# Performance work log

Measured on AMD Instinct MI355X. Metric: run time of the kernel, lower is better.

Reference implementation:

```python
import jax, jax.numpy as jnp
import numpy as np
from jax import lax

# dims
B, K, P, S = 16, 2048, 512, 16   # batch, votes, num_proposal, nsample
C = 256                           # seed_feat_dim
RADIUS = 0.3
NH, NS, PRE, TXT = 12, 10, 256, 10
HEAD_OUT = 5 + 2 * NH + 4 * NS + PRE  # conv3 out channels = 325


def setup_inputs() -> dict:
    key = jax.random.key(0)
    ks = jax.random.split(key, 16)
    w = lambda k, shp: jax.random.normal(k, shp, jnp.float32) * 0.05
    return {
        'xyz': jax.random.normal(ks[0], (B, K, 3), jnp.float32),
        'features': jax.random.normal(ks[1], (B, C, K), jnp.float32),
        'text_feats': jax.random.normal(ks[2], (TXT, 512), jnp.float32),
        # grouping MLP (1x1 conv2d, bias folded into BN)
        'g_w0': w(ks[3], (3 + C, 128)), 'g_w1': w(ks[4], (128, 128)), 'g_w2': w(ks[5], (128, 128)),
        'g_gam0': jnp.ones(128), 'g_bet0': jnp.zeros(128),
        'g_gam1': jnp.ones(128), 'g_bet1': jnp.zeros(128),
        'g_gam2': jnp.ones(128), 'g_bet2': jnp.zeros(128),
        # decode head
        'conv1_w': w(ks[6], (128, 128)), 'conv1_b': jnp.zeros(128),
        'bn1_g': jnp.ones(128), 'bn1_b': jnp.zeros(128),
        'conv2_w': w(ks[7], (128, 128)), 'conv2_b': jnp.zeros(128),
        'bn2_g': jnp.ones(128), 'bn2_b': jnp.zeros(128),
        'conv3_w': w(ks[8], (128, HEAD_OUT)), 'conv3_b': jnp.zeros(HEAD_OUT),
        # clip header
        'h_w0': w(ks[9], (PRE, 512)), 'h_b0': jnp.zeros(512), 'h_g0': jnp.ones(512), 'h_be0': jnp.zeros(512),
        'h_w1': w(ks[10], (512, 512)), 'h_b1': jnp.zeros(512), 'h_g1': jnp.ones(512), 'h_be1': jnp.zeros(512),
        'h_w2': w(ks[11], (512, 512)), 'h_b2': jnp.zeros(512),
    }


def _fps(pts):
    # farthest point sampling of P points from pts [K,3], starting at index 0
    Kp = pts.shape[0]
    def step(carry, _):
        dmin, last = carry
        d = jnp.sum((pts - pts[last]) ** 2, -1)
        dmin = jnp.minimum(dmin, d)
        nxt = jnp.argmax(dmin).astype(jnp.int32)
        return (dmin, nxt), nxt
    d0 = jnp.full((Kp,), 1e10, pts.dtype)
    _, rest = lax.scan(step, (d0, jnp.int32(0)), None, length=P - 1)
    return jnp.concatenate([jnp.zeros((1,), jnp.int32), rest])


def _bn(x, gam, bet):
    # training-mode batchnorm over all dims but channel (last)
    ax = tuple(range(x.ndim - 1))
    m = x.mean(ax, keepdims=True)
    v = x.var(ax, keepdims=True)
    return gam * (x - m) * lax.rsqrt(v + 1e-5) + bet


def reference(xyz, features, text_feats, g_w0, g_w1, g_w2, g_gam0, g_bet0, g_gam1, g_bet1, g_gam2, g_bet2, conv1_w, conv1_b, bn1_g, bn1_b, conv2_w, conv2_b, bn2_g, bn2_b, conv3_w, conv3_b, h_w0, h_b0, h_g0, h_be0, h_w1, h_b1, h_g1, h_be1, h_w2, h_b2):
    feats_kc = features.transpose(0, 2, 1)            # [B,K,C]
    inds = jax.vmap(_fps)(xyz)                        # [B,P] int32
    new_xyz = jnp.take_along_axis(xyz, inds[..., None], axis=1)  # [B,P,3]
    # ball query: first-S in-radius indices, pad with first valid (center itself)
    d2 = jnp.sum((new_xyz[:, :, None, :] - xyz[:, None, :, :]) ** 2, -1)  # [B,P,K]
    score = jnp.where(d2 < RADIUS * RADIUS, jnp.arange(K, dtype=jnp.int32), jnp.int32(K))
    neg_vals, idx = lax.top_k(-score, S)              # smallest valid indices first
    idx = jnp.where(neg_vals > -K, idx, idx[..., :1])  # [B,P,S]
    gather = jax.vmap(lambda pts, i: pts[i])
    gx = (gather(xyz, idx) - new_xyz[:, :, None, :]) / RADIUS  # normalize_xyz
    gf = gather(feats_kc, idx)
    g = jnp.concatenate([gx, gf], -1)                 # [B,P,S,3+C] (use_xyz)
    h = jax.nn.relu(_bn(g @ g_w0, g_gam0, g_bet0))
    h = jax.nn.relu(_bn(h @ g_w1, g_gam1, g_bet1))
    h = jax.nn.relu(_bn(h @ g_w2, g_gam2, g_bet2))
    feat = h.max(axis=2)                              # [B,P,128] max-pool over neighbors
    net = jax.nn.relu(_bn(feat @ conv1_w + conv1_b, bn1_g, bn1_b))
    net = jax.nn.relu(_bn(net @ conv2_w + conv2_b, bn2_g, bn2_b))
    net = net @ conv3_w + conv3_b                     # [B,P,325]
    clip_in = net[..., -PRE:]
    hh = jax.nn.relu(_bn(clip_in @ h_w0 + h_b0, h_g0, h_be0))
    hh = jax.nn.relu(_bn(hh @ h_w1 + h_b1, h_g1, h_be1))
    q = hh @ h_w2 + h_b2                              # [B,P,512]
    q = q / jnp.linalg.norm(q, axis=-1, keepdims=True)
    t = text_feats / jnp.linalg.norm(text_feats, axis=-1, keepdims=True)
    logits = (1.0 / 0.07) * jnp.einsum('bpd,td->bpt', q, t)  # logit_scale = exp(log(1/0.07))
    out = jnp.concatenate([net[..., :-PRE], logits], -1)     # [B,P,69+TXT]
    return out.transpose(0, 2, 1)                     # [B,79,P] like torch `net`
```

## Files before the change

### kernel.cpp

```cpp
#include <hip/hip_runtime.h>
#include <hip/hip_bf16.h>
#include <cstdint>
#include <cstddef>

#define Bb 16
#define Kk 2048
#define Pp 512
#define Ss 16
#define Cc 256

typedef __attribute__((ext_vector_type(8))) short bf16x8;
typedef __attribute__((ext_vector_type(4))) float f32x4;
typedef float v2f __attribute__((ext_vector_type(2)));

__device__ __forceinline__ unsigned short f2bf(float x) {
  unsigned u = __float_as_uint(x);
  u = (u + 0x7FFF + ((u >> 16) & 1)) >> 16;
  return (unsigned short)u;
}
__device__ __forceinline__ float bf2f(unsigned short s) {
  return __uint_as_float((unsigned)s << 16);
}
__device__ __forceinline__ void split2(float x, short& h, short& l) {
  unsigned u = __float_as_uint(x);
  h = (short)(u >> 16);
  float r = x - __uint_as_float(u & 0xFFFF0000u);
  l = (short)(__float_as_uint(r) >> 16);
}

static constexpr size_t OFF_TNORM = 0;
static constexpr size_t OFF_SUMS  = 20480;
static constexpr size_t OFF_INDS  = 36864;
static constexpr size_t OFF_IDXL  = 69632;
static constexpr size_t OFF_GX    = 593920;
static constexpr size_t OFF_F1    = 2166784;
static constexpr size_t OFF_BIGA  = 18944000;
static constexpr size_t OFF_BIGB  = 86052864;
static constexpr size_t OFF_NET   = 153161728;
static constexpr size_t OFF_WTH   = 155422720;
static constexpr size_t OFF_WTL   = 156962816;

#define WT_GW1 0
#define WT_GW2 16384
#define WT_C1  32768
#define WT_C2  49152
#define WT_H0  65536
#define WT_H1  196608
#define WT_H2  458752
#define WT_C3  720896

#define SB0S 0
#define SB0Q 128
#define SB1S 256
#define SB1Q 384
#define SB2S 512
#define SB2Q 640
#define SC1S 768
#define SC1Q 896
#define SC2S 1024
#define SC2Q 1152
#define SH0S 1280
#define SH0Q 1792
#define SH1S 2304
#define SH1Q 2816

template <int CTRL>
__device__ __forceinline__ float fmax_dpp(float v) {
  int o = __builtin_amdgcn_update_dpp(0, __float_as_int(v), CTRL, 0xF, 0xF, true);
  return fmaxf(v, __int_as_float(o));
}

__global__ __launch_bounds__(256, 1) void fused_pre(
    const float* __restrict__ xyz, int* __restrict__ inds,
    const float* __restrict__ features, const float* __restrict__ g_w0,
    float* __restrict__ F1, const float* __restrict__ text,
    float* __restrict__ tn, const float* __restrict__ g_w1,
    const float* __restrict__ g_w2, const float* __restrict__ conv1_w,
    const float* __restrict__ conv2_w, const float* __restrict__ conv3_w,
    const float* __restrict__ h_w0, const float* __restrict__ h_w1,
    const float* __restrict__ h_w2, unsigned short* __restrict__ wth,
    unsigned short* __restrict__ wtl) {
  __shared__ __align__(16) float smem[8208];
  const int tid = threadIdx.x;

  if (blockIdx.x < 16) {
    #pragma clang fp contract(off)
    const int b = blockIdx.x;
    float4* pt4 = (float4*)smem;
    unsigned long long (*redw)[4] = (unsigned long long(*)[4])(smem + 8192);
    const float* base = xyz + (size_t)b * Kk * 3;
    for (int i = tid; i < Kk; i += 256) {
      pt4[i] = make_float4(base[3 * i], base[3 * i + 1], base[3 * i + 2], 0.f);
    }
    if (tid == 0) inds[b * Pp] = 0;
    v2f PX[4], PY[4], PZ[4], DM[4];
    {
      const float* pb = base + tid * 24;
      float4 f0 = *(const float4*)(pb + 0);
      float4 f1 = *(const float4*)(pb + 4);
      float4 f2 = *(const float4*)(pb + 8);
      float4 f3 = *(const float4*)(pb + 12);
      float4 f4 = *(const float4*)(pb + 16);
      float4 f5 = *(const float4*)(pb + 20);
      PX[0] = (v2f){f0.x, f0.w}; PY[0] = (v2f){f0.y, f1.x}; PZ[0] = (v2f){f0.z, f1.y};
      PX[1] = (v2f){f1.z, f2.y}; PY[1] = (v2f){f1.w, f2.z}; PZ[1] = (v2f){f2.x, f2.w};
      PX[2] = (v2f){f3.x, f3.w}; PY[2] = (v2f){f3.y, f4.x}; PZ[2] = (v2f){f3.z, f4.y};
      PX[3] = (v2f){f4.z, f5.y}; PY[3] = (v2f){f4.w, f5.z}; PZ[3] = (v2f){f5.x, f5.w};
      #pragma unroll
      for (int p = 0; p < 4; p++) DM[p] = (v2f){1e10f, 1e10f};
    }
    __syncthreads();
    const int lane = tid & 63, wid = tid >> 6;
    int last = 0;
    for (int it = 1; it < Pp; ++it) {
      float4 L = pt4[last];
      v2f vlx = {L.x, L.x}, vly = {L.y, L.y}, vlz = {L.z, L.z};
      float pf[4];
      int pk_[4];
      #pragma unroll
      for (int p = 0; p < 4; p++) {
        v2f dx = PX[p] - vlx, dy = PY[p] - vly, dz = PZ[p] - vlz;
        v2f d = (dx * dx + dy * dy) + dz * dz;
        v2f m2 = __builtin_elementwise_min(DM[p], d);
        DM[p] = m2;
        bool t = m2.y > m2.x;
        pf[p] = t ? m2.y : m2.x;
        pk_[p] = 2 * p + (t ? 1 : 0);
      }
      bool t01 = pf[1] > pf[0];
      float f01 = t01 ? pf[1] : pf[0];
      int k01 = t01 ? pk_[1] : pk_[0];
      bool t23 = pf[3] > pf[2];
      float f23 = t23 ? pf[3] : pf[2];
      int k23 = t23 ? pk_[3] : pk_[2];
      bool tt = f23 > f01;
      float bf = tt ? f23 : f01;
      int bj = tt ? k23 : k01;
      float g = bf;
      g = fmax_dpp<0xB1>(g);
      g = fmax_dpp<0x4E>(g);
      g = fmax_dpp<0x141>(g);
      g = fmax_dpp<0x140>(g);
      g = fmax_dpp<0x142>(g);
      g = fmax_dpp<0x143>(g);
      float gs = __uint_as_float(
          (unsigned)__builtin_amdgcn_readlane(__float_as_int(g), 63));
      unsigned long long msk = __ballot(bf == gs);
      int src = __builtin_ctzll(msk);
      int kk = (tid << 3) | bj;
      int kwin = __builtin_amdgcn_readlane(kk, src);
      if (lane == 0)
        redw[it & 1][wid] = ((unsigned long long)__float_as_uint(gs) << 32) |
                            (unsigned)(~(unsigned)kwin);
      __syncthreads();
      unsigned long long q0 = redw[it & 1][0], q1 = redw[it & 1][1];
      unsigned long long q2 = redw[it & 1][2], q3 = redw[it & 1][3];
      unsigned long long m0 = q0 > q1 ? q0 : q1;
      unsigned long long m1 = q2 > q3 ? q2 : q3;
      unsigned long long mm = m0 > m1 ? m0 : m1;
      last = (int)(~(unsigned)mm);
      if (tid == 0) inds[b * Pp + it] = last;
    }
  } else if (blockIdx.x == 528) {
    int w = tid >> 6, lane = tid & 63;
    for (int r = w; r < 10; r += 4) {
      const float* rw = text + (size_t)r * 512;
      float v[8];
      float ss = 0.f;
      #pragma unroll
      for (int u = 0; u < 8; u++) { v[u] = rw[lane + 64 * u]; ss += v[u] * v[u]; }
      #pragma unroll
      for (int off = 32; off; off >>= 1) ss += __shfl_xor(ss, off, 64);
      float nrm = sqrtf(ss);
      #pragma unroll
      for (int u = 0; u < 8; u++)
        tn[(size_t)r * 512 + lane + 64 * u] = v[u] / nrm;
    }
  } else if (blockIdx.x >= 529) {
    int wb = blockIdx.x - 529;
    const float* W;
    int K, N, NS, nblk, pidx;
    unsigned short *dh, *dl;
    if (wb < 4)       { W = g_w1;    K = 128; N = 128; NS = 128; dh = wth + WT_GW1; dl = wtl + WT_GW1; nblk = 4;  pidx = wb; }
    else if (wb < 8)  { W = g_w2;    K = 128; N = 128; NS = 128; dh = wth + WT_GW2; dl = wtl + WT_GW2; nblk = 4;  pidx = wb - 4; }
    else if (wb < 12) { W = conv1_w; K = 128; N = 128; NS = 128; dh = wth + WT_C1;  dl = wtl + WT_C1;  nblk = 4;  pidx = wb - 8; }
    else if (wb < 16) { W = conv2_w; K = 128; N = 128; NS = 128; dh = wth + WT_C2;  dl = wtl + WT_C2;  nblk = 4;  pidx = wb - 12; }
    else if (wb < 32) { W = h_w0;    K = 256; N = 512; NS = 512; dh = wth + WT_H0;  dl = wtl + WT_H0;  nblk = 16; pidx = wb - 16; }
    else if (wb < 64) { W = h_w1;    K = 512; N = 512; NS = 512; dh = wth + WT_H1;  dl = wtl + WT_H1;  nblk = 32; pidx = wb - 32; }
    else if (wb < 96) { W = h_w2;    K = 512; N = 512; NS = 512; dh = wth + WT_H2;  dl = wtl + WT_H2;  nblk = 32; pidx = wb - 64; }
    else              { W = conv3_w; K = 128; N = 384; NS = 325; dh = wth + WT_C3;  dl = wtl + WT_C3;  nblk = 4;  pidx = wb - 96; }
    for (int idx = pidx * 256 + tid; idx < K * N; idx += nblk * 256) {
      int k = idx / N, n = idx - k * N;
      float w = (n < NS) ? W[k * NS + n] : 0.f;
      unsigned short hi = f2bf(w);
      unsigned short lo = f2bf(w - bf2f(hi));
      dh[n * K + k] = hi;
      dl[n * K + k] = lo;
    }
  } else {
    float (*a_t)[68] = (float(*)[68])smem;
    float (*b_t)[128] = (float(*)[128])(smem + 32 * 68);
    const float* W = g_w0 + 3 * 128;
    const int m0 = (blockIdx.x - 16) * 64;
    float acc[4][8];
    #pragma unroll
    for (int i = 0; i < 4; i++)
      #pragma unroll
      for (int j = 0; j < 8; j++) acc[i][j] = 0.f;
    const int ty = tid >> 4, tx = tid & 15;
    const int lr = tid & 63, wv = tid >> 6;
    const int bb = m0 >> 11, k0 = m0 & 2047;
    const float* fb = features + (size_t)bb * (Cc * Kk);
    for (int c0 = 0; c0 < 256; c0 += 32) {
      #pragma unroll
      for (int i = 0; i < 8; i++) {
        int c = c0 + wv + 4 * i;
        a_t[wv + 4 * i][lr] = fb[(size_t)c * Kk + k0 + lr];
      }
      #pragma unroll
      for (int p = 0; p < 4; p++) {
        int cc = p * 8 + (tid >> 5);
        int nl = (tid & 31) * 4;
        *(float4*)&b_t[cc][nl] = *(const float4*)&W[(size_t)(c0 + cc) * 128 + nl];
      }
      __syncthreads();
      #pragma unroll
      for (int kk = 0; kk < 32; kk++) {
        float4 av = *(const float4*)&a_t[kk][ty * 4];
        float4 b0 = *(const float4*)&b_t[kk][tx * 4];
        float4 b1 = *(const float4*)&b_t[kk][tx * 4 + 64];
        float ap[4] = {av.x, av.y, av.z, av.w};
        float bq0[4] = {b0.x, b0.y, b0.z, b0.w};
        float bq1[4] = {b1.x, b1.y, b1.z, b1.w};
        #pragma unroll
        for (int i = 0; i < 4; i++) {
          #pragma unroll
          for (int u = 0; u < 4; u++) {
            acc[i][u] = fmaf(ap[i], bq0[u], acc[i][u]);
            acc[i][4 + u] = fmaf(ap[i], bq1[u], acc[i][4 + u]);
          }
        }
      }
      __syncthreads();
    }
    #pragma unroll
    for (int i = 0; i < 4; i++) {
      size_t mrow = (size_t)(m0 + ty * 4 + i);
      #pragma unroll
      for (int gq = 0; gq < 2; gq++) {
        float4 v4 = make_float4(acc[i][gq * 4], acc[i][gq * 4 + 1],
                                acc[i][gq * 4 + 2], acc[i][gq * 4 + 3]);
        *(float4*)&F1[mrow * 128 + gq * 64 + tx * 4] = v4;
      }
    }
  }
}

__global__ __launch_bounds__(256) void neigh_k(
    const float* __restrict__ xyz, const int* __restrict__ inds,
    const float* __restrict__ F1, const float* __restrict__ g_w0,
    int* __restrict__ idxl, float* __restrict__ gx, float* __restrict__ s0,
    float* __restrict__ q0) {
  __shared__ float rs[128], rq[128];
  const int tid = threadIdx.x;
  if (tid < 128) { rs[tid] = 0.f; rq[tid] = 0.f; }
  __syncthreads();
  int widx = blockIdx.x * 4 + (tid >> 6);
  int lane = tid & 63;
  int b = widx >> 9;
  int q = inds[widx];
  const float* base = xyz + (size_t)b * Kk * 3;
  float qx = base[3 * q], qy = base[3 * q + 1], qz = base[3 * q + 2];
  int cnt = 0;
  int myk = 0;
  for (int ch = 0; ch < 32 && cnt < Ss; ch++) {
    int k = ch * 64 + lane;
    float dx = base[3 * k] - qx;
    float dy = base[3 * k + 1] - qy;
    float dz = base[3 * k + 2] - qz;
    float d2 = __fadd_rn(__fadd_rn(__fmul_rn(dx, dx), __fmul_rn(dy, dy)),
                         __fmul_rn(dz, dz));
    unsigned long long m = __ballot(d2 < 0.09f);
    while (m && cnt < Ss) {
      int t = __builtin_ctzll(m);
      if (lane == cnt) myk = ch * 64 + t;
      cnt++;
      m &= m - 1;
    }
  }
  int first = __shfl(myk, 0, 64);
  int kksel = 0;
  float g0r = 0.f, g1r = 0.f, g2r = 0.f;
  if (lane < Ss) {
    int kk = (lane < cnt) ? myk : first;
    kksel = kk;
    g0r = (base[3 * kk] - qx) / 0.3f;
    g1r = (base[3 * kk + 1] - qy) / 0.3f;
    g2r = (base[3 * kk + 2] - qz) / 0.3f;
    size_t o = (size_t)widx * Ss + lane;
    idxl[o] = kk;
    gx[o * 3 + 0] = g0r;
    gx[o * 3 + 1] = g1r;
    gx[o * 3 + 2] = g2r;
  }
  const float* f1b = F1 + (size_t)(b << 11) * 128;
  float wa0 = g_w0[lane], wa1 = g_w0[128 + lane], wa2 = g_w0[256 + lane];
  float wb0 = g_w0[64 + lane], wb1 = g_w0[192 + lane], wb2 = g_w0[320 + lane];
  float sa = 0.f, qa = 0.f, sb = 0.f, qb = 0.f;
  #pragma unroll
  for (int s = 0; s < Ss; s++) {
    int bidx = __shfl(kksel, s, 64);
    float gg0 = __shfl(g0r, s, 64);
    float gg1 = __shfl(g1r, s, 64);
    float gg2 = __shfl(g2r, s, 64);
    const float* fr = f1b + (size_t)bidx * 128;
    float va = fr[lane] + gg0 * wa0 + gg1 * wa1 + gg2 * wa2;
    float vb = fr[64 + lane] + gg0 * wb0 + gg1 * wb1 + gg2 * wb2;
    sa += va; qa += va * va;
    sb += vb; qb += vb * vb;
  }
  atomicAdd(&rs[lane], sa);
  atomicAdd(&rq[lane], qa);
  atomicAdd(&rs[64 + lane], sb);
  atomicAdd(&rq[64 + lane], qb);
  __syncthreads();
  if (tid < 128) {
    atomicAdd(&s0[tid], rs[tid]);
    atomicAdd(&q0[tid], rq[tid]);
  }
}

template <int KD, bool INBN, bool HASBIAS, bool OSUM, bool OMAX, bool WCLIP,
          bool ABF16, bool GATHER, bool OBF16>
__global__ __launch_bounds__(256, 2) void gemm_mfma(
    const void* __restrict__ A, const unsigned short* __restrict__ Wh,
    const unsigned short* __restrict__ Wl, const float* __restrict__ bias,
    const float* __restrict__ isum, const float* __restrict__ isq,
    float inv_cnt, const float* __restrict__ gamma,
    const float* __restrict__ beta, void* __restrict__ outp, int N, int nout,
    float* __restrict__ clipf, float* __restrict__ osum,
    float* __restrict__ osq, const int* __restrict__ idxl,
    const float* __restrict__ gxv, const float* __restrict__ w0raw) {
  __shared__ float sc[INBN ? KD : 1];
  __shared__ float sh[INBN ? KD : 1];
  __shared__ float red_s[OSUM ? 128 : 1];
  __shared__ float red_q[OSUM ? 128 : 1];
  const int tid = threadIdx.x;
  if (INBN) {
    for (int c = tid; c < KD; c += 256) {
      float mean = isum[c] * inv_cnt;
      float var = isq[c] * inv_cnt - mean * mean;
      float is_ = rsqrtf(var + 1e-5f);
      float scl = gamma[c] * is_;
      sc[c] = scl;
      sh[c] = beta[c] - mean * scl;
    }
  }
  if (OSUM && tid < 128) { red_s[tid] = 0.f; red_q[tid] = 0.f; }
  __syncthreads();
  const int wave = tid >> 6, lane = tid & 63;
  const int wm = wave >> 1, wn = wave & 1;
  const int r = lane & 15, g = lane >> 4;
  const size_t m0 = (size_t)blockIdx.x * 128 + wm * 64;
  const int n0 = blockIdx.y * 128 + wn * 64;

  const float* Af = (const float*)A;
  const unsigned short* Ab = (const unsigned short*)A;

  size_t gi[4];
  float gx0[4], gx1[4], gx2[4];
  if (GATHER) {
    #pragma unroll
    for (int mf = 0; mf < 4; mf++) {
      int row = (int)m0 + mf * 16 + r;
      gi[mf] = ((size_t)((row >> 13) << 11) + idxl[row]) * 128;
      gx0[mf] = gxv[3 * (size_t)row];
      gx1[mf] = gxv[3 * (size_t)row + 1];
      gx2[mf] = gxv[3 * (size_t)row + 2];
    }
  }

  f32x4 acc[4][4] = {};
  for (int ks = 0; ks < KD / 32; ks++) {
    const int kb = ks * 32 + g * 8;
    bf16x8 bh[4], bl[4];
    #pragma unroll
    for (int nf = 0; nf < 4; nf++) {
      bh[nf] = *(const bf16x8*)&Wh[(size_t)(n0 + nf * 16 + r) * KD + kb];
      bl[nf] = *(const bf16x8*)&Wl[(size_t)(n0 + nf * 16 + r) * KD + kb];
    }
    float s8[8], h8[8];
    if (INBN) {
      #pragma unroll
      for (int j = 0; j < 8; j++) { s8[j] = sc[kb + j]; h8[j] = sh[kb + j]; }
    }
    float wxr[8], wyr[8], wzr[8];
    if (GATHER) {
      float4 a0 = *(const float4*)&w0raw[kb];
      float4 a1 = *(const float4*)&w0raw[kb + 4];
      float4 b0 = *(const float4*)&w0raw[128 + kb];
      float4 b1 = *(const float4*)&w0raw[128 + kb + 4];
      float4 c0 = *(const float4*)&w0raw[256 + kb];
      float4 c1 = *(const float4*)&w0raw[256 + kb + 4];
      wxr[0]=a0.x; wxr[1]=a0.y; wxr[2]=a0.z; wxr[3]=a0.w;
      wxr[4]=a1.x; wxr[5]=a1.y; wxr[6]=a1.z; wxr[7]=a1.w;
      wyr[0]=b0.x; wyr[1]=b0.y; wyr[2]=b0.z; wyr[3]=b0.w;
      wyr[4]=b1.x; wyr[5]=b1.y; wyr[6]=b1.z; wyr[7]=b1.w;
      wzr[0]=c0.x; wzr[1]=c0.y; wzr[2]=c0.z; wzr[3]=c0.w;
      wzr[4]=c1.x; wzr[5]=c1.y; wzr[6]=c1.z; wzr[7]=c1.w;
    }
    #pragma unroll
    for (int mf = 0; mf < 4; mf++) {
      float xv[8];
      if (GATHER) {
        const float* fp = Af + gi[mf] + kb;
        float4 x0 = *(const float4*)fp;
        float4 x1 = *(const float4*)(fp + 4);
        xv[0]=x0.x; xv[1]=x0.y; xv[2]=x0.z; xv[3]=x0.w;
        xv[4]=x1.x; xv[5]=x1.y; xv[6]=x1.z; xv[7]=x1.w;
        #pragma unroll
        for (int j = 0; j < 8; j++)
          xv[j] += gx0[mf] * wxr[j] + gx1[mf] * wyr[j] + gx2[mf] * wzr[j];
      } else if (ABF16) {
        bf16x8 rawv = *(const bf16x8*)&Ab[(m0 + mf * 16 + r) * KD + kb];
        #pragma unroll
        for (int j = 0; j < 8; j++) xv[j] = bf2f((unsigned short)rawv[j]);
      } else {
        const float* ap = Af + (m0 + mf * 16 + r) * KD + kb;
        float4 x0 = *(const float4*)ap;
        float4 x1 = *(const float4*)(ap + 4);
        xv[0]=x0.x; xv[1]=x0.y; xv[2]=x0.z; xv[3]=x0.w;
        xv[4]=x1.x; xv[5]=x1.y; xv[6]=x1.z; xv[7]=x1.w;
      }
      bf16x8 ah, al;
      #pragma unroll
      for (int j = 0; j < 8; j++) {
        float x = xv[j];
        if (INBN) x = fmaxf(fmaf(x, s8[j], h8[j]), 0.f);
        short hh, ll;
        split2(x, hh, ll);
        ah[j] = hh;
        al[j] = ll;
      }
      #pragma unroll
      for (int nf = 0; nf < 4; nf++) {
        acc[mf][nf] = __builtin_amdgcn_mfma_f32_16x16x32_bf16(
            ah, bh[nf], acc[mf][nf], 0, 0, 0);
        acc[mf][nf] = __builtin_amdgcn_mfma_f32_16x16x32_bf16(
            al, bh[nf], acc[mf][nf], 0, 0, 0);
        acc[mf][nf] = __builtin_amdgcn_mfma_f32_16x16x32_bf16(
            ah, bl[nf], acc[mf][nf], 0, 0, 0);
      }
    }
  }
  float bv[4];
  if (HASBIAS) {
    #pragma unroll
    for (int nf = 0; nf < 4; nf++) {
      int col = n0 + nf * 16 + r;
      bv[nf] = (!WCLIP || col < nout) ? bias[col] : 0.f;
    }
  }
  float ps[4] = {0.f, 0.f, 0.f, 0.f}, pq[4] = {0.f, 0.f, 0.f, 0.f};
  #pragma unroll
  for (int mf = 0; mf < 4; mf++) {
    float mx[4];
    #pragma unroll
    for (int nf = 0; nf < 4; nf++) {
      float vmax = -1e30f;
      #pragma unroll
      for (int j = 0; j < 4; j++) {
        float v = acc[mf][nf][j];
        if (HASBIAS) v += bv[nf];
        size_t row = m0 + mf * 16 + g * 4 + j;
        int col = n0 + nf * 16 + r;
        if (OSUM) { ps[nf] += v; pq[nf] += v * v; }
        if (OMAX) {
          vmax = fmaxf(vmax, v);
        } else if (WCLIP) {
          if (col < 69) ((float*)outp)[row * 69 + col] = v;
          else if (col < nout) clipf[row * 256 + (col - 69)] = v;
        } else if (OBF16) {
          ((unsigned short*)outp)[row * N + col] = f2bf(v);
        } else {
          ((float*)outp)[row * N + col] = v;
        }
      }
      mx[nf] = vmax;
    }
    if (OMAX) {
      #pragma unroll
      for (int nf = 0; nf < 4; nf++) {
        float m = mx[nf];
        m = fmaxf(m, __shfl_xor(m, 16, 64));
        m = fmaxf(m, __shfl_xor(m, 32, 64));
        if (g == 0) {
          size_t bq = (m0 >> 4) + mf;
          ((float*)outp)[bq * 128 + n0 + nf * 16 + r] = m;
        }
      }
    }
  }
  if (OSUM) {
    #pragma unroll
    for (int nf = 0; nf < 4; nf++) {
      #pragma unroll
      for (int off = 16; off < 64; off <<= 1) {
        ps[nf] += __shfl_xor(ps[nf], off, 64);
        pq[nf] += __shfl_xor(pq[nf], off, 64);
      }
    }
    if (lane < 16) {
      #pragma unroll
      for (int nf = 0; nf < 4; nf++) {
        int lcol = wn * 64 + nf * 16 + r;
        atomicAdd(&red_s[lcol], ps[nf]);
        atomicAdd(&red_q[lcol], pq[nf]);
      }
    }
    __syncthreads();
    if (tid < 128) {
      atomicAdd(&osum[blockIdx.y * 128 + tid], red_s[tid]);
      atomicAdd(&osq[blockIdx.y * 128 + tid], red_q[tid]);
    }
  }
}

__global__ __launch_bounds__(512) void final2(const float* __restrict__ net,
                                              const float* __restrict__ qbuf,
                                              const float* __restrict__ tn,
                                              float* __restrict__ out) {
  __shared__ float tile[79][65];
  const int blk = blockIdx.x;
  const int tid = threadIdx.x;
  const int r = tid >> 3, oct = tid & 7;
  const int row = blk * 64 + r;
  const int b = (blk * 64) >> 9, p0 = (blk * 64) & 511;

  const float* qr = qbuf + (size_t)row * 512 + oct * 64;
  float4 q4[16];
  #pragma unroll
  for (int i = 0; i < 16; i++) q4[i] = *(const float4*)(qr + 4 * i);
  float ss = 0.f;
  float dot[10];
  #pragma unroll
  for (int t = 0; t < 10; t++) dot[t] = 0.f;
  #pragma unroll
  for (int i = 0; i < 16; i++) {
    float4 a = q4[i];
    ss += a.x * a.x + a.y * a.y + a.z * a.z + a.w * a.w;
    #pragma unroll
    for (int t = 0; t < 10; t++) {
      float4 b4 = *(const float4*)(tn + (size_t)t * 512 + oct * 64 + i * 4);
      dot[t] += a.x * b4.x + a.y * b4.y + a.z * b4.z + a.w * b4.w;
    }
  }
  #pragma unroll
  for (int off = 1; off < 8; off <<= 1) {
    ss += __shfl_xor(ss, off, 8);
    #pragma unroll
    for (int t = 0; t < 10; t++) dot[t] += __shfl_xor(dot[t], off, 8);
  }
  if (oct == 0) {
    float inv = rsqrtf(ss) * (1.f / 0.07f);
    #pragma unroll
    for (int t = 0; t < 10; t++) tile[69 + t][r] = dot[t] * inv;
  }
  for (int idx = tid; idx < 64 * 69; idx += 512) {
    int r2 = idx / 69, ch = idx - 69 * r2;
    tile[ch][r2] = net[(size_t)(blk * 64 + r2) * 69 + ch];
  }
  __syncthreads();
  for (int idx = tid; idx < 79 * 64; idx += 512) {
    int ch = idx >> 6, rr = idx & 63;
    out[((size_t)b * 79 + ch) * 512 + p0 + rr] = tile[ch][rr];
  }
}

extern "C" void kernel_launch(void* const* d_in, const int* in_sizes, int n_in,
                              void* d_out, int out_size, void* d_ws,
                              size_t ws_size, hipStream_t stream) {
  const float* xyz = (const float*)d_in[0];
  const float* features = (const float*)d_in[1];
  const float* text = (const float*)d_in[2];
  const float* g_w0 = (const float*)d_in[3];
  const float* g_w1 = (const float*)d_in[4];
  const float* g_w2 = (const float*)d_in[5];
  const float* g_gam0 = (const float*)d_in[6];
  const float* g_bet0 = (const float*)d_in[7];
  const float* g_gam1 = (const float*)d_in[8];
  const float* g_bet1 = (const float*)d_in[9];
  const float* g_gam2 = (const float*)d_in[10];
  const float* g_bet2 = (const float*)d_in[11];
  const float* conv1_w = (const float*)d_in[12];
  const float* conv1_b = (const float*)d_in[13];
  const float* bn1_g = (const float*)d_in[14];
  const float* bn1_b = (const float*)d_in[15];
  const float* conv2_w = (const float*)d_in[16];
  const float* conv2_b = (const float*)d_in[17];
  const float* bn2_g = (const float*)d_in[18];
  const float* bn2_b = (const float*)d_in[19];
  const float* conv3_w = (const float*)d_in[20];
  const float* conv3_b = (const float*)d_in[21];
  const float* h_w0 = (const float*)d_in[22];
  const float* h_b0 = (const float*)d_in[23];
  const float* h_g0 = (const float*)d_in[24];
  const float* h_be0 = (const float*)d_in[25];
  const float* h_w1 = (const float*)d_in[26];
  const float* h_b1 = (const float*)d_in[27];
  const float* h_g1 = (const float*)d_in[28];
  const float* h_be1 = (const float*)d_in[29];
  const float* h_w2 = (const float*)d_in[30];
  const float* h_b2 = (const float*)d_in[31];
  float* out = (float*)d_out;
  char* ws = (char*)d_ws;

  float* tn = (float*)(ws + OFF_TNORM);
  float* sums = (float*)(ws + OFF_SUMS);
  int* inds = (int*)(ws + OFF_INDS);
  int* idxl = (int*)(ws + OFF_IDXL);
  float* gx = (float*)(ws + OFF_GX);
  float* F1 = (float*)(ws + OFF_F1);
  unsigned short* L2OUT = (unsigned short*)(ws + OFF_BIGA);
  float* QF = (float*)(ws + OFF_BIGA);
  float* FEAT = (float*)(ws + OFF_BIGB);
  float* C1F = (float*)(ws + OFF_BIGB + 4194304);
  float* C2F = (float*)(ws + OFF_BIGB + 8388608);
  float* CLIPF = (float*)(ws + OFF_BIGB + 12582912);
  float* H0F = (float*)(ws + OFF_BIGB + 20971520);
  float* H1F = (float*)(ws + OFF_BIGB + 37748736);
  float* net = (float*)(ws + OFF_NET);
  unsigned short* WTH = (unsigned short*)(ws + OFF_WTH);
  unsigned short* WTL = (unsigned short*)(ws + OFF_WTL);

  hipMemsetAsync(sums, 0, 16384, stream);
  fused_pre<<<629, 256, 0, stream>>>(xyz, inds, features, g_w0, F1, text, tn,
                                     g_w1, g_w2, conv1_w, conv2_w, conv3_w,
                                     h_w0, h_w1, h_w2, WTH, WTL);
  neigh_k<<<2048, 256, 0, stream>>>(xyz, inds, F1, g_w0, idxl, gx,
                                    sums + SB0S, sums + SB0Q);
  gemm_mfma<128, true, false, true, false, false, false, true, true>
      <<<dim3(1024, 1), 256, 0, stream>>>(
          F1, WTH + WT_GW1, WTL + WT_GW1, nullptr, sums + SB0S, sums + SB0Q,
          1.f / 131072.f, g_gam0, g_bet0, L2OUT, 128, 128, nullptr,
          sums + SB1S, sums + SB1Q, idxl, gx, g_w0);
  gemm_mfma<128, true, false, true, true, false, true, false, false>
      <<<dim3(1024, 1), 256, 0, stream>>>(
          L2OUT, WTH + WT_GW2, WTL + WT_GW2, nullptr, sums + SB1S,
          sums + SB1Q, 1.f / 131072.f, g_gam1, g_bet1, FEAT, 128, 128,
          nullptr, sums + SB2S, sums + SB2Q, nullptr, nullptr, nullptr);
  gemm_mfma<128, true, true, true, false, false, false, false, false>
      <<<dim3(64, 1), 256, 0, stream>>>(
          FEAT, WTH + WT_C1, WTL + WT_C1, conv1_b, sums + SB2S, sums + SB2Q,
          1.f / 131072.f, g_gam2, g_bet2, C1F, 128, 128, nullptr, sums + SC1S,
          sums + SC1Q, nullptr, nullptr, nullptr);
  gemm_mfma<128, true, true, true, false, false, false, false, false>
      <<<dim3(64, 1), 256, 0, stream>>>(
          C1F, WTH + WT_C2, WTL + WT_C2, conv2_b, sums + SC1S, sums + SC1Q,
          1.f / 8192.f, bn1_g, bn1_b, C2F, 128, 128, nullptr, sums + SC2S,
          sums + SC2Q, nullptr, nullptr, nullptr);
  gemm_mfma<128, true, true, false, false, true, false, false, false>
      <<<dim3(64, 3), 256, 0, stream>>>(
          C2F, WTH + WT_C3, WTL + WT_C3, conv3_b, sums + SC2S, sums + SC2Q,
          1.f / 8192.f, bn2_g, bn2_b, net, 384, 325, CLIPF, nullptr, nullptr,
          nullptr, nullptr, nullptr);
  gemm_mfma<256, false, true, true, false, false, false, false, false>
      <<<dim3(64, 4), 256, 0, stream>>>(
          CLIPF, WTH + WT_H0, WTL + WT_H0, h_b0, nullptr, nullptr, 0.f,
          nullptr, nullptr, H0F, 512, 512, nullptr, sums + SH0S, sums + SH0Q,
          nullptr, nullptr, nullptr);
  gemm_mfma<512, true, true, true, false, false, false, false, false>
      <<<dim3(64, 4), 256, 0, stream>>>(
          H0F, WTH + WT_H1, WTL + WT_H1, h_b1, sums + SH0S, sums + SH0Q,
          1.f / 8192.f, h_g0, h_be0, H1F, 512, 512, nullptr, sums + SH1S,
          sums + SH1Q, nullptr, nullptr, nullptr);
  gemm_mfma<512, true, true, false, false, false, false, false, false>
      <<<dim3(64, 4), 256, 0, stream>>>(
          H1F, WTH + WT_H2, WTL + WT_H2, h_b2, sums + SH1S, sums + SH1Q,
          1.f / 8192.f, h_g1, h_be1, QF, 512, 512, nullptr, nullptr, nullptr,
          nullptr, nullptr, nullptr);
  final2<<<128, 512, 0, stream>>>(net, QF, tn, out);
}
```

Before: 749.7 us.

## Carry FPS winner coordinates through reduction; stage xyz in LDS for ball query

In the FPS blocks, the winning lane now publishes its point's coordinates alongside the packed distance/index key, so the next iteration takes the new query point from the reduction instead of an LDS lookup table. This drops the upfront xyz-to-shared-memory fill and the dependent LDS load on the serial critical path. The ball-query kernel now stages the batch's xyz points into shared memory as float4 and reads neighbours from there instead of strided global loads. Each neighbour block repeats a 2048-point load and uses 32KB of LDS, which may lower occupancy.

```diff
diff --git a/kernel.cpp b/kernel.cpp
--- a/kernel.cpp
+++ b/kernel.cpp
@@ -86,12 +86,9 @@
   if (blockIdx.x < 16) {
     #pragma clang fp contract(off)
     const int b = blockIdx.x;
-    float4* pt4 = (float4*)smem;
-    unsigned long long (*redw)[4] = (unsigned long long(*)[4])(smem + 8192);
+    unsigned long long (*redk)[4] = (unsigned long long(*)[4])smem;
+    float4 (*redc)[4] = (float4(*)[4])(smem + 16);
     const float* base = xyz + (size_t)b * Kk * 3;
-    for (int i = tid; i < Kk; i += 256) {
-      pt4[i] = make_float4(base[3 * i], base[3 * i + 1], base[3 * i + 2], 0.f);
-    }
     if (tid == 0) inds[b * Pp] = 0;
     v2f PX[4], PY[4], PZ[4], DM[4];
     {
@@ -109,12 +106,10 @@
       #pragma unroll
       for (int p = 0; p < 4; p++) DM[p] = (v2f){1e10f, 1e10f};
     }
-    __syncthreads();
+    float lx = base[0], ly = base[1], lz = base[2];
     const int lane = tid & 63, wid = tid >> 6;
-    int last = 0;
     for (int it = 1; it < Pp; ++it) {
-      float4 L = pt4[last];
-      v2f vlx = {L.x, L.x}, vly = {L.y, L.y}, vlz = {L.z, L.z};
+      v2f vlx = {lx, lx}, vly = {ly, ly}, vlz = {lz, lz};
       float pf[4];
       int pk_[4];
       #pragma unroll
@@ -147,19 +142,32 @@
           (unsigned)__builtin_amdgcn_readlane(__float_as_int(g), 63));
       unsigned long long msk = __ballot(bf == gs);
       int src = __builtin_ctzll(msk);
-      int kk = (tid << 3) | bj;
-      int kwin = __builtin_amdgcn_readlane(kk, src);
-      if (lane == 0)
-        redw[it & 1][wid] = ((unsigned long long)__float_as_uint(gs) << 32) |
-                            (unsigned)(~(unsigned)kwin);
+      if (lane == src) {
+        int p = bj >> 1;
+        float wx = (bj & 1) ? PX[p].y : PX[p].x;
+        float wy = (bj & 1) ? PY[p].y : PY[p].x;
+        float wz = (bj & 1) ? PZ[p].y : PZ[p].x;
+        int kk = (tid << 3) | bj;
+        redk[it & 1][wid] = ((unsigned long long)__float_as_uint(gs) << 32) |
+                            (unsigned)(~(unsigned)kk);
+        redc[it & 1][wid] = make_float4(wx, wy, wz, 0.f);
+      }
       __syncthreads();
-      unsigned long long q0 = redw[it & 1][0], q1 = redw[it & 1][1];
-      unsigned long long q2 = redw[it & 1][2], q3 = redw[it & 1][3];
-      unsigned long long m0 = q0 > q1 ? q0 : q1;
-      unsigned long long m1 = q2 > q3 ? q2 : q3;
-      unsigned long long mm = m0 > m1 ? m0 : m1;
-      last = (int)(~(unsigned)mm);
-      if (tid == 0) inds[b * Pp + it] = last;
+      unsigned long long q0 = redk[it & 1][0], q1 = redk[it & 1][1];
+      unsigned long long q2 = redk[it & 1][2], q3 = redk[it & 1][3];
+      float4 c0 = redc[it & 1][0], c1 = redc[it & 1][1];
+      float4 c2 = redc[it & 1][2], c3 = redc[it & 1][3];
+      bool s01 = q0 > q1;
+      unsigned long long m01 = s01 ? q0 : q1;
+      float4 cc01 = s01 ? c0 : c1;
+      bool s23 = q2 > q3;
+      unsigned long long m23 = s23 ? q2 : q3;
+      float4 cc23 = s23 ? c2 : c3;
+      bool sw = m23 > m01;
+      unsigned long long mm = sw ? m23 : m01;
+      float4 cw = sw ? cc23 : cc01;
+      lx = cw.x; ly = cw.y; lz = cw.z;
+      if (tid == 0) inds[b * Pp + it] = (int)(~(unsigned)mm);
     }
   } else if (blockIdx.x == 528) {
     int w = tid >> 6, lane = tid & 63;
@@ -262,22 +270,26 @@
     int* __restrict__ idxl, float* __restrict__ gx, float* __restrict__ s0,
     float* __restrict__ q0) {
   __shared__ float rs[128], rq[128];
+  __shared__ __align__(16) float4 pts[Kk];
   const int tid = threadIdx.x;
   if (tid < 128) { rs[tid] = 0.f; rq[tid] = 0.f; }
-  __syncthreads();
   int widx = blockIdx.x * 4 + (tid >> 6);
   int lane = tid & 63;
   int b = widx >> 9;
+  const float* base = xyz + (size_t)b * Kk * 3;
+  for (int i = tid; i < Kk; i += 256)
+    pts[i] = make_float4(base[3 * i], base[3 * i + 1], base[3 * i + 2], 0.f);
+  __syncthreads();
   int q = inds[widx];
-  const float* base = xyz + (size_t)b * Kk * 3;
-  float qx = base[3 * q], qy = base[3 * q + 1], qz = base[3 * q + 2];
+  float4 Q = pts[q];
+  float qx = Q.x, qy = Q.y, qz = Q.z;
   int cnt = 0;
   int myk = 0;
   for (int ch = 0; ch < 32 && cnt < Ss; ch++) {
-    int k = ch * 64 + lane;
-    float dx = base[3 * k] - qx;
-    float dy = base[3 * k + 1] - qy;
-    float dz = base[3 * k + 2] - qz;
+    float4 P = pts[ch * 64 + lane];
+    float dx = P.x - qx;
+    float dy = P.y - qy;
+    float dz = P.z - qz;
     float d2 = __fadd_rn(__fadd_rn(__fmul_rn(dx, dx), __fmul_rn(dy, dy)),
                          __fmul_rn(dz, dz));
     unsigned long long m = __ballot(d2 < 0.09f);
@@ -294,9 +306,10 @@
   if (lane < Ss) {
     int kk = (lane < cnt) ? myk : first;
     kksel = kk;
-    g0r = (base[3 * kk] - qx) / 0.3f;
-    g1r = (base[3 * kk + 1] - qy) / 0.3f;
-    g2r = (base[3 * kk + 2] - qz) / 0.3f;
+    float4 P = pts[kk];
+    g0r = (P.x - qx) / 0.3f;
+    g1r = (P.y - qy) / 0.3f;
+    g2r = (P.z - qz) / 0.3f;
     size_t o = (size_t)widx * Ss + lane;
     idxl[o] = kk;
     gx[o * 3 + 0] = g0r;
```

New measurement: 838.5 us. 1.12x slower.
